# Performance work log

Hardware: AMD Instinct MI355X
Metric: run time of the kernel (lower is better)

Reference implementation:

```python
import jax, jax.numpy as jnp
import numpy as np

N_NODES = 50000
N_EDGES = 640000
NFEAT = 128
NHID = 128
BN_EPS = 1e-5
GIN_EPS = 0.0  # GINConv default eps


def setup_inputs() -> dict:
    key = jax.random.key(0)
    ks = jax.random.split(key, 8)
    x = jax.random.normal(ks[0], (N_NODES, NFEAT), dtype=jnp.float32)
    edge_index = jax.random.randint(ks[1], (2, N_EDGES), 0, N_NODES, dtype=jnp.int64)
    # xavier-uniform linears, zero bias (per weights_init); BN gamma=1, beta=0
    def xavier(k, fan_in, fan_out):
        a = float(np.sqrt(6.0 / (fan_in + fan_out)))
        return jax.random.uniform(k, (fan_in, fan_out), dtype=jnp.float32, minval=-a, maxval=a)
    W1 = xavier(ks[2], NFEAT, NHID)
    b1 = jnp.zeros((NHID,), dtype=jnp.float32)
    gamma = jnp.ones((NHID,), dtype=jnp.float32)
    beta = jnp.zeros((NHID,), dtype=jnp.float32)
    W2 = xavier(ks[3], NHID, NHID)
    b2 = jnp.zeros((NHID,), dtype=jnp.float32)
    return {"x": x, "edge_index": edge_index, "W1": W1, "b1": b1,
            "gamma": gamma, "beta": beta, "W2": W2, "b2": b2}


def reference(x, edge_index, W1, b1, gamma, beta, W2, b2):
    src, dst = edge_index[0], edge_index[1]
    # sparse neighbor sum-aggregation: agg[i] = sum_{(src->dst=i)} x[src]
    agg = jax.ops.segment_sum(x[src], dst, num_segments=x.shape[0])
    h = (1.0 + GIN_EPS) * x + agg
    # MLP: Linear -> ReLU -> BatchNorm1d (training-mode batch stats) -> Linear
    h = jax.nn.relu(h @ W1 + b1)
    mean = jnp.mean(h, axis=0)
    var = jnp.mean(jnp.square(h - mean), axis=0)  # biased var, as torch BN uses
    h = (h - mean) * jax.lax.rsqrt(var + BN_EPS) * gamma + beta
    return h @ W2 + b2
```

## Files before the change

kernel.cpp:

```cpp
#include <hip/hip_runtime.h>
#include <hip/hip_fp16.h>

#define NNODES 50000
#define NEDGES 640000
#define NF 128
#define XB 3125
#define WB 64
#define BINS 196
#define BINCAP 4096
#define P1B 625

typedef __attribute__((ext_vector_type(8))) _Float16 f16x8;
typedef __attribute__((ext_vector_type(4))) float f32x4;

__global__ __launch_bounds__(256) void k_prep(const float* __restrict__ x,
                                              const float* __restrict__ W1,
                                              const int* __restrict__ ei,
                                              unsigned short* __restrict__ xh,
                                              _Float16* __restrict__ wp1,
                                              int* __restrict__ gcursor,
                                              unsigned* __restrict__ binbuf,
                                              float* __restrict__ stats) {
  __shared__ int lcnt[BINS], lbase[BINS];
  const int bid = blockIdx.x, t = threadIdx.x;
  if (bid < XB) {
    int i = bid * 256 + t;
    const float4 a = ((const float4*)x)[2 * i];
    const float4 b = ((const float4*)x)[2 * i + 1];
    __half2 h0 = __float22half2_rn(make_float2(a.x, a.y));
    __half2 h1 = __float22half2_rn(make_float2(a.z, a.w));
    __half2 h2 = __float22half2_rn(make_float2(b.x, b.y));
    __half2 h3 = __float22half2_rn(make_float2(b.z, b.w));
    uint4 v;
    v.x = *(unsigned*)&h0; v.y = *(unsigned*)&h1;
    v.z = *(unsigned*)&h2; v.w = *(unsigned*)&h3;
    ((uint4*)xh)[i] = v;
    if (bid == 0) { stats[t] = 0.f; stats[256 + t] = 0.f; }
  } else if (bid < XB + WB) {
    int f = (bid - XB) * 256 + t;
    int j = f & 7, lane = (f >> 3) & 63, cf = (f >> 9) & 7, ks = f >> 12;
    int k = ks * 32 + ((lane >> 4) << 3) + j;
    int n = cf * 16 + (lane & 15);
    float w = W1[k * NF + n];
    _Float16 hi = (_Float16)w;
    _Float16 lo = (_Float16)(w - (float)hi);
    wp1[f] = hi;
    wp1[16384 + f] = lo;
  } else {
    const int e0 = (bid - (XB + WB)) * 1024;
    const int4 s4 = *(const int4*)(ei + e0 + 4 * t);
    const int4 d4 = *(const int4*)(ei + NEDGES + e0 + 4 * t);
    if (t < BINS) lcnt[t] = 0;
    __syncthreads();
    atomicAdd(&lcnt[d4.x >> 8], 1);
    atomicAdd(&lcnt[d4.y >> 8], 1);
    atomicAdd(&lcnt[d4.z >> 8], 1);
    atomicAdd(&lcnt[d4.w >> 8], 1);
    __syncthreads();
    if (t < BINS) {
      lbase[t] = atomicAdd(&gcursor[t], lcnt[t]);
      lcnt[t] = 0;
    }
    __syncthreads();
    {
      int bin = d4.x >> 8;
      int idx = lbase[bin] + atomicAdd(&lcnt[bin], 1);
      if (idx < BINCAP) binbuf[bin * BINCAP + idx] = ((unsigned)(d4.x & 255) << 16) | (unsigned)s4.x;
    }
    {
      int bin = d4.y >> 8;
      int idx = lbase[bin] + atomicAdd(&lcnt[bin], 1);
      if (idx < BINCAP) binbuf[bin * BINCAP + idx] = ((unsigned)(d4.y & 255) << 16) | (unsigned)s4.y;
    }
    {
      int bin = d4.z >> 8;
      int idx = lbase[bin] + atomicAdd(&lcnt[bin], 1);
      if (idx < BINCAP) binbuf[bin * BINCAP + idx] = ((unsigned)(d4.z & 255) << 16) | (unsigned)s4.z;
    }
    {
      int bin = d4.w >> 8;
      int idx = lbase[bin] + atomicAdd(&lcnt[bin], 1);
      if (idx < BINCAP) binbuf[bin * BINCAP + idx] = ((unsigned)(d4.w & 255) << 16) | (unsigned)s4.w;
    }
  }
}

__global__ __launch_bounds__(256) void k_p2(const unsigned* __restrict__ binbuf,
                                            const int* __restrict__ gcursor,
                                            int* __restrict__ begdeg,
                                            unsigned short* __restrict__ slot) {
  __shared__ int cnt2[256], pst[256];
  __shared__ unsigned short stg[BINCAP];
  const int t = threadIdx.x;
  const int b = blockIdx.x;
  const int base = b * BINCAP;
  const int nb = min(gcursor[b], BINCAP);
  unsigned pk[16];
#pragma unroll
  for (int ci = 0; ci < 16; ++ci) {
    int i = (ci << 8) + t;
    pk[ci] = (i < nb) ? binbuf[base + i] : 0xFFFFFFFFu;
  }
  cnt2[t] = 0;
  __syncthreads();
#pragma unroll
  for (int ci = 0; ci < 16; ++ci)
    if (pk[ci] != 0xFFFFFFFFu) atomicAdd(&cnt2[(int)(pk[ci] >> 16)], 1);
  __syncthreads();
  pst[t] = cnt2[t];
  __syncthreads();
  for (int d = 1; d < 256; d <<= 1) {
    int u = (t >= d) ? pst[t - d] : 0;
    __syncthreads();
    pst[t] += u;
    __syncthreads();
  }
  pst[t] -= cnt2[t];
  int node = (b << 8) + t;
  if (node < NNODES)
    begdeg[node] = ((base + pst[t]) << 8) | min(cnt2[t], 255);
  cnt2[t] = 0;
  __syncthreads();
#pragma unroll
  for (int ci = 0; ci < 16; ++ci)
    if (pk[ci] != 0xFFFFFFFFu) {
      int dl = (int)(pk[ci] >> 16);
      int pos = atomicAdd(&cnt2[dl], 1);
      stg[pst[dl] + pos] = (unsigned short)(pk[ci] & 0xffffu);
    }
  __syncthreads();
  for (int i = t; i < nb; i += 256) slot[base + i] = stg[i];
}

__device__ inline void add8h(float* a, uint4 v) {
  const __half2* p = (const __half2*)&v;
#pragma unroll
  for (int q = 0; q < 4; ++q) {
    float2 f = __half22float2(p[q]);
    a[2 * q] += f.x;
    a[2 * q + 1] += f.y;
  }
}

__global__ __launch_bounds__(256) void k_gather(const unsigned short* __restrict__ xh,
                                                const int* __restrict__ begdeg,
                                                const unsigned short* __restrict__ slot,
                                                _Float16* __restrict__ h) {
  const int t = threadIdx.x;
  const int wv = t >> 6, l = t & 63;
  const int node = blockIdx.x * 4 + wv;
  if (node >= NNODES) return;
  const int cg = (l & 15) << 3;
  const int e = l >> 4;
  const int bd = begdeg[node];
  const int beg = bd >> 8;
  const int end = beg + (bd & 255);
  float a[8] = {0.f, 0.f, 0.f, 0.f, 0.f, 0.f, 0.f, 0.f};
  float b[8] = {0.f, 0.f, 0.f, 0.f, 0.f, 0.f, 0.f, 0.f};
  int j = beg + e;
  for (; j + 4 < end; j += 8) {
    const uint4 v0 = *(const uint4*)(xh + (size_t)slot[j] * NF + cg);
    const uint4 v1 = *(const uint4*)(xh + (size_t)slot[j + 4] * NF + cg);
    add8h(a, v0);
    add8h(b, v1);
  }
  if (j < end) {
    const uint4 v0 = *(const uint4*)(xh + (size_t)slot[j] * NF + cg);
    add8h(a, v0);
  }
#pragma unroll
  for (int q = 0; q < 8; ++q) a[q] += b[q];
#pragma unroll
  for (int q = 0; q < 8; ++q) {
    a[q] += __shfl_xor(a[q], 16);
    a[q] += __shfl_xor(a[q], 32);
  }
  if (e == 0) {
    const uint4 sv = *(const uint4*)(xh + (size_t)node * NF + cg);
    add8h(a, sv);
    f16x8 o;
#pragma unroll
    for (int q = 0; q < 8; ++q) o[q] = (_Float16)a[q];
    *(f16x8*)(h + (size_t)node * NF + cg) = o;
  }
}

template <int MODE>
__global__ __launch_bounds__(256, 2) void k_gemm(const _Float16* __restrict__ A,
                                                 const _Float16* __restrict__ wprep,
                                                 const float* __restrict__ bias,
                                                 float* __restrict__ stats,
                                                 _Float16* __restrict__ outh,
                                                 float* __restrict__ outf) {
  __shared__ _Float16 wl[32768];
  __shared__ float red[2][4][128];

  const int t = threadIdx.x;
  const int wv = t >> 6;
  const int l = t & 63;
  const int wrow0 = blockIdx.x * 128 + wv * 16;

  f16x8 areg[2][4];
#pragma unroll
  for (int m = 0; m < 2; ++m) {
    const int arow = wrow0 + m * 64 + (l & 15);
    const bool okA = arow < NNODES;
#pragma unroll
    for (int ks = 0; ks < 4; ++ks) {
      if (okA) {
        areg[m][ks] = *(const f16x8*)(A + (size_t)arow * NF + ks * 32 + ((l >> 4) << 3));
      } else {
        areg[m][ks] = (f16x8){};
      }
    }
  }

  const float4* src = (const float4*)wprep;
#pragma unroll
  for (int it = 0; it < 16; ++it) {
    ((float4*)wl)[it * 256 + t] = src[it * 256 + t];
  }
  __syncthreads();

  f32x4 acc[2][8];
#pragma unroll
  for (int m = 0; m < 2; ++m)
#pragma unroll
    for (int cf = 0; cf < 8; ++cf) acc[m][cf] = (f32x4){0.f, 0.f, 0.f, 0.f};

#pragma unroll
  for (int ks = 0; ks < 4; ++ks) {
#pragma unroll
    for (int cf = 0; cf < 8; ++cf) {
      const int fo = (((ks * 8 + cf) << 6) + l) << 3;
      f16x8 bh = *(const f16x8*)(wl + fo);
      f16x8 bl = *(const f16x8*)(wl + 16384 + fo);
#pragma unroll
      for (int m = 0; m < 2; ++m) {
        acc[m][cf] = __builtin_amdgcn_mfma_f32_16x16x32_f16(areg[m][ks], bh, acc[m][cf], 0, 0, 0);
        acc[m][cf] = __builtin_amdgcn_mfma_f32_16x16x32_f16(areg[m][ks], bl, acc[m][cf], 0, 0, 0);
      }
    }
  }

  const int col16 = l & 15;
  const int rg = l >> 4;
  float bl_[8];
#pragma unroll
  for (int cf = 0; cf < 8; ++cf) bl_[cf] = bias[cf * 16 + col16];

  if (MODE == 0) {
    float cs[8], cq[8];
#pragma unroll
    for (int cf = 0; cf < 8; ++cf) { cs[cf] = 0.f; cq[cf] = 0.f; }
#pragma unroll
    for (int m = 0; m < 2; ++m)
#pragma unroll
      for (int cf = 0; cf < 8; ++cf) {
#pragma unroll
        for (int r = 0; r < 4; ++r) {
          int row = wrow0 + m * 64 + rg * 4 + r;
          if (row < NNODES) {
            float v = fmaxf(acc[m][cf][r] + bl_[cf], 0.f);
            outh[(size_t)row * NF + cf * 16 + col16] = (_Float16)v;
            cs[cf] += v;
            cq[cf] += v * v;
          }
        }
      }
#pragma unroll
    for (int cf = 0; cf < 8; ++cf) {
      cs[cf] += __shfl_xor(cs[cf], 16); cs[cf] += __shfl_xor(cs[cf], 32);
      cq[cf] += __shfl_xor(cq[cf], 16); cq[cf] += __shfl_xor(cq[cf], 32);
    }
    if (l < 16) {
#pragma unroll
      for (int cf = 0; cf < 8; ++cf) {
        red[0][wv][cf * 16 + l] = cs[cf];
        red[1][wv][cf * 16 + l] = cq[cf];
      }
    }
    __syncthreads();
    if (t < 128) {
      float s = red[0][0][t] + red[0][1][t] + red[0][2][t] + red[0][3][t];
      float q = red[1][0][t] + red[1][1][t] + red[1][2][t] + red[1][3][t];
      unsafeAtomicAdd(stats + t, s);
      unsafeAtomicAdd(stats + 128 + t, q);
    }
  } else {
#pragma unroll
    for (int m = 0; m < 2; ++m)
#pragma unroll
      for (int cf = 0; cf < 8; ++cf) {
#pragma unroll
        for (int r = 0; r < 4; ++r) {
          int row = wrow0 + m * 64 + rg * 4 + r;
          if (row < NNODES)
            outf[(size_t)row * NF + cf * 16 + col16] = acc[m][cf][r] + bl_[cf];
        }
      }
  }
}

__global__ __launch_bounds__(1024) void k_bnfold(const float* __restrict__ stats,
                                                 const float* __restrict__ gamma,
                                                 const float* __restrict__ beta,
                                                 const float* __restrict__ W2,
                                                 const float* __restrict__ b2,
                                                 _Float16* __restrict__ wp2,
                                                 float* __restrict__ b2p) {
  __shared__ float sc_s[128], sh_s[128];
  __shared__ float part[8][128];
  const int t = threadIdx.x;
  if (t < 128) {
    const float inv = 1.0f / (float)NNODES;
    float mean = stats[t] * inv;
    float var = stats[128 + t] * inv - mean * mean;
    var = fmaxf(var, 0.f);
    float sc = gamma[t] * rsqrtf(var + 1e-5f);
    sc_s[t] = sc;
    sh_s[t] = beta[t] - mean * sc;
  }
  __syncthreads();
#pragma unroll
  for (int it = 0; it < 16; ++it) {
    int f = it * 1024 + t;
    int j = f & 7, lane = (f >> 3) & 63, cf = (f >> 9) & 7, ks = f >> 12;
    int k = ks * 32 + ((lane >> 4) << 3) + j;
    int n = cf * 16 + (lane & 15);
    float w = sc_s[k] * W2[k * NF + n];
    _Float16 hi = (_Float16)w;
    _Float16 lo = (_Float16)(w - (float)hi);
    wp2[f] = hi;
    wp2[16384 + f] = lo;
  }
  {
    const int col = t & 127, ch = t >> 7;
    float s = 0.f;
    for (int k = ch * 16; k < ch * 16 + 16; ++k) s += sh_s[k] * W2[k * NF + col];
    part[ch][col] = s;
  }
  __syncthreads();
  if (t < 128) {
    float v = b2[t];
#pragma unroll
    for (int c = 0; c < 8; ++c) v += part[c][t];
    b2p[t] = v;
  }
}

extern "C" void kernel_launch(void* const* d_in, const int* in_sizes, int n_in,
                              void* d_out, int out_size, void* d_ws, size_t ws_size,
                              hipStream_t stream) {
  const float* x     = (const float*)d_in[0];
  const int*   ei    = (const int*)d_in[1];
  const float* W1    = (const float*)d_in[2];
  const float* b1    = (const float*)d_in[3];
  const float* gamma = (const float*)d_in[4];
  const float* beta  = (const float*)d_in[5];
  const float* W2    = (const float*)d_in[6];
  const float* b2    = (const float*)d_in[7];
  float* out = (float*)d_out;

  _Float16* h = (_Float16*)d_out;

  float*          stats   = (float*)d_ws;
  _Float16*       wp1     = (_Float16*)(stats + 512);
  _Float16*       wp2     = wp1 + 32768;
  float*          b2p     = (float*)(wp2 + 32768);
  int*            gcursor = (int*)(b2p + 128);
  int*            begdeg  = gcursor + 256;
  unsigned*       binbuf  = (unsigned*)(begdeg + 50176);
  unsigned short* slot    = (unsigned short*)(binbuf + BINS * BINCAP);
  unsigned short* xh      = slot + BINS * BINCAP;
  _Float16*       h1      = (_Float16*)(xh + (size_t)NNODES * NF);

  hipMemsetAsync(gcursor, 0, 256 * sizeof(int), stream);
  k_prep   <<<XB + WB + P1B, 256, 0, stream>>>(x, W1, ei, xh, wp1, gcursor, binbuf, stats);
  k_p2     <<<BINS, 256, 0, stream>>>(binbuf, gcursor, begdeg, slot);
  k_gather <<<(NNODES + 3) / 4, 256, 0, stream>>>(xh, begdeg, slot, h);
  k_gemm<0><<<(NNODES + 127) / 128, 256, 0, stream>>>(h, wp1, b1, stats, h1, nullptr);
  k_bnfold <<<1, 1024, 0, stream>>>(stats, gamma, beta, W2, b2, wp2, b2p);
  k_gemm<1><<<(NNODES + 127) / 128, 256, 0, stream>>>(h1, wp2, b2p, nullptr, nullptr, out);
}
```

Baseline: 105.3 us.

## Replace global-atomic edge binning with count/scan/scatter passes; parallelize BN fold

The edge binning step no longer reserves space per bin with global atomics on a shared cursor. It now writes per-block bin counts, runs a per-bin exclusive scan across blocks in a new kernel, and then scatters the edges in a third kernel using the precomputed offsets. This removes the memset and global atomic contention, and it makes the bin order deterministic. The cost is two extra kernel launches and a second read of the edge indices. The BN-fold kernel is also split from one 1024-thread block into 17 blocks, which spreads the weight repacking across more compute units.

```diff
diff --git a/kernel.cpp b/kernel.cpp
--- a/kernel.cpp
+++ b/kernel.cpp
@@ -8,7 +8,8 @@
 #define WB 64
 #define BINS 196
 #define BINCAP 4096
-#define P1B 625
+#define P1AB 313
+#define EPB 2048
 
 typedef __attribute__((ext_vector_type(8))) _Float16 f16x8;
 typedef __attribute__((ext_vector_type(4))) float f32x4;
@@ -18,10 +19,9 @@
                                               const int* __restrict__ ei,
                                               unsigned short* __restrict__ xh,
                                               _Float16* __restrict__ wp1,
-                                              int* __restrict__ gcursor,
-                                              unsigned* __restrict__ binbuf,
+                                              int* __restrict__ cnt,
                                               float* __restrict__ stats) {
-  __shared__ int lcnt[BINS], lbase[BINS];
+  __shared__ int lcnt[BINS];
   const int bid = blockIdx.x, t = threadIdx.x;
   if (bid < XB) {
     int i = bid * 256 + t;
@@ -47,46 +47,75 @@
     wp1[f] = hi;
     wp1[16384 + f] = lo;
   } else {
-    const int e0 = (bid - (XB + WB)) * 1024;
-    const int4 s4 = *(const int4*)(ei + e0 + 4 * t);
-    const int4 d4 = *(const int4*)(ei + NEDGES + e0 + 4 * t);
+    const int blk = bid - (XB + WB);
+    const int e0 = blk * EPB;
+    const bool full = (e0 + EPB <= NEDGES);
     if (t < BINS) lcnt[t] = 0;
     __syncthreads();
-    atomicAdd(&lcnt[d4.x >> 8], 1);
-    atomicAdd(&lcnt[d4.y >> 8], 1);
-    atomicAdd(&lcnt[d4.z >> 8], 1);
-    atomicAdd(&lcnt[d4.w >> 8], 1);
-    __syncthreads();
-    if (t < BINS) {
-      lbase[t] = atomicAdd(&gcursor[t], lcnt[t]);
-      lcnt[t] = 0;
-    }
-    __syncthreads();
-    {
-      int bin = d4.x >> 8;
-      int idx = lbase[bin] + atomicAdd(&lcnt[bin], 1);
-      if (idx < BINCAP) binbuf[bin * BINCAP + idx] = ((unsigned)(d4.x & 255) << 16) | (unsigned)s4.x;
-    }
-    {
-      int bin = d4.y >> 8;
-      int idx = lbase[bin] + atomicAdd(&lcnt[bin], 1);
-      if (idx < BINCAP) binbuf[bin * BINCAP + idx] = ((unsigned)(d4.y & 255) << 16) | (unsigned)s4.y;
-    }
-    {
-      int bin = d4.z >> 8;
-      int idx = lbase[bin] + atomicAdd(&lcnt[bin], 1);
-      if (idx < BINCAP) binbuf[bin * BINCAP + idx] = ((unsigned)(d4.z & 255) << 16) | (unsigned)s4.z;
-    }
-    {
-      int bin = d4.w >> 8;
-      int idx = lbase[bin] + atomicAdd(&lcnt[bin], 1);
-      if (idx < BINCAP) binbuf[bin * BINCAP + idx] = ((unsigned)(d4.w & 255) << 16) | (unsigned)s4.w;
-    }
-  }
+    const int4 d0 = *(const int4*)(ei + NEDGES + e0 + 4 * t);
+    atomicAdd(&lcnt[d0.x >> 8], 1);
+    atomicAdd(&lcnt[d0.y >> 8], 1);
+    atomicAdd(&lcnt[d0.z >> 8], 1);
+    atomicAdd(&lcnt[d0.w >> 8], 1);
+    if (full) {
+      const int4 d1 = *(const int4*)(ei + NEDGES + e0 + 1024 + 4 * t);
+      atomicAdd(&lcnt[d1.x >> 8], 1);
+      atomicAdd(&lcnt[d1.y >> 8], 1);
+      atomicAdd(&lcnt[d1.z >> 8], 1);
+      atomicAdd(&lcnt[d1.w >> 8], 1);
+    }
+    __syncthreads();
+    if (t < BINS) cnt[blk * BINS + t] = lcnt[t];
+  }
+}
+
+__global__ __launch_bounds__(512) void k_p1b(const int* __restrict__ cnt,
+                                             int* __restrict__ base,
+                                             int* __restrict__ gtot) {
+  __shared__ int s[512];
+  const int t = threadIdx.x, b = blockIdx.x;
+  const int v = (t < P1AB) ? cnt[t * BINS + b] : 0;
+  s[t] = v;
+  __syncthreads();
+  for (int d = 1; d < 512; d <<= 1) {
+    int u = (t >= d) ? s[t - d] : 0;
+    __syncthreads();
+    s[t] += u;
+    __syncthreads();
+  }
+  if (t < P1AB) base[t * BINS + b] = s[t] - v;
+  if (t == 511) gtot[b] = s[511];
+}
+
+__global__ __launch_bounds__(256) void k_p1c(const int* __restrict__ ei,
+                                             const int* __restrict__ base,
+                                             unsigned* __restrict__ binbuf) {
+  __shared__ int lcur[BINS];
+  const int t = threadIdx.x, blk = blockIdx.x;
+  const int e0 = blk * EPB;
+  const bool full = (e0 + EPB <= NEDGES);
+  if (t < BINS) lcur[t] = base[blk * BINS + t];
+  __syncthreads();
+  const int4 s0 = *(const int4*)(ei + e0 + 4 * t);
+  const int4 d0 = *(const int4*)(ei + NEDGES + e0 + 4 * t);
+#define SCAT(ss, dd)                                                             \
+  {                                                                              \
+    int bin = (dd) >> 8;                                                         \
+    int pos = atomicAdd(&lcur[bin], 1);                                          \
+    if (pos < BINCAP)                                                            \
+      binbuf[bin * BINCAP + pos] = ((unsigned)((dd) & 255) << 16) | (unsigned)(ss); \
+  }
+  SCAT(s0.x, d0.x); SCAT(s0.y, d0.y); SCAT(s0.z, d0.z); SCAT(s0.w, d0.w);
+  if (full) {
+    const int4 s1 = *(const int4*)(ei + e0 + 1024 + 4 * t);
+    const int4 d1 = *(const int4*)(ei + NEDGES + e0 + 1024 + 4 * t);
+    SCAT(s1.x, d1.x); SCAT(s1.y, d1.y); SCAT(s1.z, d1.z); SCAT(s1.w, d1.w);
+  }
+#undef SCAT
 }
 
 __global__ __launch_bounds__(256) void k_p2(const unsigned* __restrict__ binbuf,
-                                            const int* __restrict__ gcursor,
+                                            const int* __restrict__ gtot,
                                             int* __restrict__ begdeg,
                                             unsigned short* __restrict__ slot) {
   __shared__ int cnt2[256], pst[256];
@@ -94,7 +123,7 @@
   const int t = threadIdx.x;
   const int b = blockIdx.x;
   const int base = b * BINCAP;
-  const int nb = min(gcursor[b], BINCAP);
+  const int nb = min(gtot[b], BINCAP);
   unsigned pk[16];
 #pragma unroll
   for (int ci = 0; ci < 16; ++ci) {
@@ -302,16 +331,16 @@
   }
 }
 
-__global__ __launch_bounds__(1024) void k_bnfold(const float* __restrict__ stats,
-                                                 const float* __restrict__ gamma,
-                                                 const float* __restrict__ beta,
-                                                 const float* __restrict__ W2,
-                                                 const float* __restrict__ b2,
-                                                 _Float16* __restrict__ wp2,
-                                                 float* __restrict__ b2p) {
+__global__ __launch_bounds__(256) void k_fold(const float* __restrict__ stats,
+                                              const float* __restrict__ gamma,
+                                              const float* __restrict__ beta,
+                                              const float* __restrict__ W2,
+                                              const float* __restrict__ b2,
+                                              _Float16* __restrict__ wp2,
+                                              float* __restrict__ b2p) {
   __shared__ float sc_s[128], sh_s[128];
-  __shared__ float part[8][128];
-  const int t = threadIdx.x;
+  __shared__ float part[2][128];
+  const int t = threadIdx.x, bb = blockIdx.x;
   if (t < 128) {
     const float inv = 1.0f / (float)NNODES;
     float mean = stats[t] * inv;
@@ -322,30 +351,26 @@
     sh_s[t] = beta[t] - mean * sc;
   }
   __syncthreads();
-#pragma unroll
-  for (int it = 0; it < 16; ++it) {
-    int f = it * 1024 + t;
-    int j = f & 7, lane = (f >> 3) & 63, cf = (f >> 9) & 7, ks = f >> 12;
-    int k = ks * 32 + ((lane >> 4) << 3) + j;
-    int n = cf * 16 + (lane & 15);
-    float w = sc_s[k] * W2[k * NF + n];
-    _Float16 hi = (_Float16)w;
-    _Float16 lo = (_Float16)(w - (float)hi);
-    wp2[f] = hi;
-    wp2[16384 + f] = lo;
-  }
-  {
+  if (bb < 16) {
+#pragma unroll
+    for (int it = 0; it < 4; ++it) {
+      int f = bb * 1024 + it * 256 + t;
+      int j = f & 7, lane = (f >> 3) & 63, cf = (f >> 9) & 7, ks = f >> 12;
+      int k = ks * 32 + ((lane >> 4) << 3) + j;
+      int n = cf * 16 + (lane & 15);
+      float w = sc_s[k] * W2[k * NF + n];
+      _Float16 hi = (_Float16)w;
+      _Float16 lo = (_Float16)(w - (float)hi);
+      wp2[f] = hi;
+      wp2[16384 + f] = lo;
+    }
+  } else {
     const int col = t & 127, ch = t >> 7;
     float s = 0.f;
-    for (int k = ch * 16; k < ch * 16 + 16; ++k) s += sh_s[k] * W2[k * NF + col];
+    for (int k = ch * 64; k < ch * 64 + 64; ++k) s += sh_s[k] * W2[k * NF + col];
     part[ch][col] = s;
-  }
-  __syncthreads();
-  if (t < 128) {
-    float v = b2[t];
-#pragma unroll
-    for (int c = 0; c < 8; ++c) v += part[c][t];
-    b2p[t] = v;
+    __syncthreads();
+    if (t < 128) b2p[t] = b2[t] + part[0][t] + part[1][t];
   }
 }
 
@@ -364,22 +389,25 @@
 
   _Float16* h = (_Float16*)d_out;
 
-  float*          stats   = (float*)d_ws;
-  _Float16*       wp1     = (_Float16*)(stats + 512);
-  _Float16*       wp2     = wp1 + 32768;
-  float*          b2p     = (float*)(wp2 + 32768);
-  int*            gcursor = (int*)(b2p + 128);
-  int*            begdeg  = gcursor + 256;
-  unsigned*       binbuf  = (unsigned*)(begdeg + 50176);
-  unsigned short* slot    = (unsigned short*)(binbuf + BINS * BINCAP);
-  unsigned short* xh      = slot + BINS * BINCAP;
-  _Float16*       h1      = (_Float16*)(xh + (size_t)NNODES * NF);
-
-  hipMemsetAsync(gcursor, 0, 256 * sizeof(int), stream);
-  k_prep   <<<XB + WB + P1B, 256, 0, stream>>>(x, W1, ei, xh, wp1, gcursor, binbuf, stats);
-  k_p2     <<<BINS, 256, 0, stream>>>(binbuf, gcursor, begdeg, slot);
+  float*          stats  = (float*)d_ws;
+  _Float16*       wp1    = (_Float16*)(stats + 512);
+  _Float16*       wp2    = wp1 + 32768;
+  float*          b2p    = (float*)(wp2 + 32768);
+  int*            cnt    = (int*)(b2p + 128);
+  int*            basep  = cnt + 61376;
+  int*            gtot   = basep + 61376;
+  int*            begdeg = gtot + 256;
+  unsigned*       binbuf = (unsigned*)(begdeg + 50176);
+  unsigned short* slot   = (unsigned short*)(binbuf + BINS * BINCAP);
+  unsigned short* xh     = slot + BINS * BINCAP;
+  _Float16*       h1     = (_Float16*)(xh + (size_t)NNODES * NF);
+
+  k_prep   <<<XB + WB + P1AB, 256, 0, stream>>>(x, W1, ei, xh, wp1, cnt, stats);
+  k_p1b    <<<BINS, 512, 0, stream>>>(cnt, basep, gtot);
+  k_p1c    <<<P1AB, 256, 0, stream>>>(ei, basep, binbuf);
+  k_p2     <<<BINS, 256, 0, stream>>>(binbuf, gtot, begdeg, slot);
   k_gather <<<(NNODES + 3) / 4, 256, 0, stream>>>(xh, begdeg, slot, h);
   k_gemm<0><<<(NNODES + 127) / 128, 256, 0, stream>>>(h, wp1, b1, stats, h1, nullptr);
-  k_bnfold <<<1, 1024, 0, stream>>>(stats, gamma, beta, W2, b2, wp2, b2p);
+  k_fold   <<<17, 256, 0, stream>>>(stats, gamma, beta, W2, b2, wp2, b2p);
   k_gemm<1><<<(NNODES + 127) / 128, 256, 0, stream>>>(h1, wp2, b2p, nullptr, nullptr, out);
 }
```

New measurement: 90.56 us. 14.0% less time.

## Replace atomic edge binning with count-scan-scatter cooperative sort and fold weight prep into GEMMs

Applied to the files above, without the earlier changes.

Edge binning now counts per-block bin histograms in the prep kernel, then runs a single cooperative kernel. That kernel scans the counts, scatters edges to fixed per-block offsets and does the per-bin CSR build, separated by grid syncs. This replaces the global atomic cursors, the memset and the separate k_p2 launch. The W1/W2 fp16 hi/lo packing and the BatchNorm fold are moved into each GEMM block, which removes the standalone prep work and the single-block k_bnfold launch. In exchange, every GEMM block redundantly converts the full weight matrix from fp32, and the second GEMM also recomputes the folded bias serially. The change also depends on cooperative launch and grid-wide barriers.

```diff
diff --git a/kernel.cpp b/kernel.cpp
--- a/kernel.cpp
+++ b/kernel.cpp
@@ -1,27 +1,27 @@
 #include <hip/hip_runtime.h>
 #include <hip/hip_fp16.h>
+#include <hip/hip_cooperative_groups.h>
+
+namespace cg = cooperative_groups;
 
 #define NNODES 50000
 #define NEDGES 640000
 #define NF 128
 #define XB 3125
-#define WB 64
 #define BINS 196
 #define BINCAP 4096
-#define P1B 625
+#define P1AB 250
+#define EPB 2560
 
 typedef __attribute__((ext_vector_type(8))) _Float16 f16x8;
 typedef __attribute__((ext_vector_type(4))) float f32x4;
 
 __global__ __launch_bounds__(256) void k_prep(const float* __restrict__ x,
-                                              const float* __restrict__ W1,
                                               const int* __restrict__ ei,
                                               unsigned short* __restrict__ xh,
-                                              _Float16* __restrict__ wp1,
-                                              int* __restrict__ gcursor,
-                                              unsigned* __restrict__ binbuf,
+                                              int* __restrict__ cnt,
                                               float* __restrict__ stats) {
-  __shared__ int lcnt[BINS], lbase[BINS];
+  __shared__ int lcnt[BINS];
   const int bid = blockIdx.x, t = threadIdx.x;
   if (bid < XB) {
     int i = bid * 256 + t;
@@ -36,100 +36,101 @@
     v.z = *(unsigned*)&h2; v.w = *(unsigned*)&h3;
     ((uint4*)xh)[i] = v;
     if (bid == 0) { stats[t] = 0.f; stats[256 + t] = 0.f; }
-  } else if (bid < XB + WB) {
-    int f = (bid - XB) * 256 + t;
-    int j = f & 7, lane = (f >> 3) & 63, cf = (f >> 9) & 7, ks = f >> 12;
-    int k = ks * 32 + ((lane >> 4) << 3) + j;
-    int n = cf * 16 + (lane & 15);
-    float w = W1[k * NF + n];
-    _Float16 hi = (_Float16)w;
-    _Float16 lo = (_Float16)(w - (float)hi);
-    wp1[f] = hi;
-    wp1[16384 + f] = lo;
   } else {
-    const int e0 = (bid - (XB + WB)) * 1024;
-    const int4 s4 = *(const int4*)(ei + e0 + 4 * t);
-    const int4 d4 = *(const int4*)(ei + NEDGES + e0 + 4 * t);
+    const int blk = bid - XB;
+    const int e0 = blk * EPB;
     if (t < BINS) lcnt[t] = 0;
     __syncthreads();
-    atomicAdd(&lcnt[d4.x >> 8], 1);
-    atomicAdd(&lcnt[d4.y >> 8], 1);
-    atomicAdd(&lcnt[d4.z >> 8], 1);
-    atomicAdd(&lcnt[d4.w >> 8], 1);
-    __syncthreads();
-    if (t < BINS) {
-      lbase[t] = atomicAdd(&gcursor[t], lcnt[t]);
-      lcnt[t] = 0;
-    }
-    __syncthreads();
-    {
-      int bin = d4.x >> 8;
-      int idx = lbase[bin] + atomicAdd(&lcnt[bin], 1);
-      if (idx < BINCAP) binbuf[bin * BINCAP + idx] = ((unsigned)(d4.x & 255) << 16) | (unsigned)s4.x;
-    }
-    {
-      int bin = d4.y >> 8;
-      int idx = lbase[bin] + atomicAdd(&lcnt[bin], 1);
-      if (idx < BINCAP) binbuf[bin * BINCAP + idx] = ((unsigned)(d4.y & 255) << 16) | (unsigned)s4.y;
-    }
-    {
-      int bin = d4.z >> 8;
-      int idx = lbase[bin] + atomicAdd(&lcnt[bin], 1);
-      if (idx < BINCAP) binbuf[bin * BINCAP + idx] = ((unsigned)(d4.z & 255) << 16) | (unsigned)s4.z;
-    }
-    {
-      int bin = d4.w >> 8;
-      int idx = lbase[bin] + atomicAdd(&lcnt[bin], 1);
-      if (idx < BINCAP) binbuf[bin * BINCAP + idx] = ((unsigned)(d4.w & 255) << 16) | (unsigned)s4.w;
-    }
-  }
-}
-
-__global__ __launch_bounds__(256) void k_p2(const unsigned* __restrict__ binbuf,
-                                            const int* __restrict__ gcursor,
-                                            int* __restrict__ begdeg,
-                                            unsigned short* __restrict__ slot) {
+    for (int i = t; i < EPB; i += 256)
+      atomicAdd(&lcnt[ei[NEDGES + e0 + i] >> 8], 1);
+    __syncthreads();
+    if (t < BINS) cnt[blk * BINS + t] = lcnt[t];
+  }
+}
+
+__global__ __launch_bounds__(256) void k_sort(const int* __restrict__ ei,
+                                              const int* __restrict__ cnt,
+                                              int* __restrict__ base,
+                                              unsigned* __restrict__ binbuf,
+                                              int* __restrict__ begdeg,
+                                              unsigned short* __restrict__ slot) {
+  __shared__ int sbuf[256];
+  __shared__ int lcur[BINS];
+  __shared__ int nb_sh;
   __shared__ int cnt2[256], pst[256];
   __shared__ unsigned short stg[BINCAP];
-  const int t = threadIdx.x;
-  const int b = blockIdx.x;
-  const int base = b * BINCAP;
-  const int nb = min(gcursor[b], BINCAP);
-  unsigned pk[16];
-#pragma unroll
-  for (int ci = 0; ci < 16; ++ci) {
-    int i = (ci << 8) + t;
-    pk[ci] = (i < nb) ? binbuf[base + i] : 0xFFFFFFFFu;
-  }
-  cnt2[t] = 0;
-  __syncthreads();
-#pragma unroll
-  for (int ci = 0; ci < 16; ++ci)
-    if (pk[ci] != 0xFFFFFFFFu) atomicAdd(&cnt2[(int)(pk[ci] >> 16)], 1);
-  __syncthreads();
-  pst[t] = cnt2[t];
-  __syncthreads();
-  for (int d = 1; d < 256; d <<= 1) {
-    int u = (t >= d) ? pst[t - d] : 0;
-    __syncthreads();
-    pst[t] += u;
-    __syncthreads();
-  }
-  pst[t] -= cnt2[t];
-  int node = (b << 8) + t;
-  if (node < NNODES)
-    begdeg[node] = ((base + pst[t]) << 8) | min(cnt2[t], 255);
-  cnt2[t] = 0;
-  __syncthreads();
-#pragma unroll
-  for (int ci = 0; ci < 16; ++ci)
-    if (pk[ci] != 0xFFFFFFFFu) {
-      int dl = (int)(pk[ci] >> 16);
-      int pos = atomicAdd(&cnt2[dl], 1);
-      stg[pst[dl] + pos] = (unsigned short)(pk[ci] & 0xffffu);
-    }
-  __syncthreads();
-  for (int i = t; i < nb; i += 256) slot[base + i] = stg[i];
+  cg::grid_group grid = cg::this_grid();
+  const int t = threadIdx.x, b = blockIdx.x;
+
+  if (b < BINS) {
+    int v = (t < P1AB) ? cnt[t * BINS + b] : 0;
+    sbuf[t] = v;
+    __syncthreads();
+    for (int d = 1; d < 256; d <<= 1) {
+      int u = (t >= d) ? sbuf[t - d] : 0;
+      __syncthreads();
+      sbuf[t] += u;
+      __syncthreads();
+    }
+    if (t < P1AB) base[t * BINS + b] = sbuf[t] - v;
+    if (t == 255) nb_sh = sbuf[255];
+  }
+  grid.sync();
+
+  {
+    const int e0 = b * EPB;
+    if (t < BINS) lcur[t] = base[b * BINS + t];
+    __syncthreads();
+    for (int i = t; i < EPB; i += 256) {
+      int s = ei[e0 + i];
+      int d = ei[NEDGES + e0 + i];
+      int bin = d >> 8;
+      int pos = atomicAdd(&lcur[bin], 1);
+      if (pos < BINCAP)
+        binbuf[bin * BINCAP + pos] = ((unsigned)(d & 255) << 16) | (unsigned)s;
+    }
+  }
+  grid.sync();
+
+  if (b < BINS) {
+    const int basei = b * BINCAP;
+    const int nb = min(nb_sh, BINCAP);
+    unsigned pk[16];
+#pragma unroll
+    for (int ci = 0; ci < 16; ++ci) {
+      int i = (ci << 8) + t;
+      pk[ci] = (i < nb) ? binbuf[basei + i] : 0xFFFFFFFFu;
+    }
+    cnt2[t] = 0;
+    __syncthreads();
+#pragma unroll
+    for (int ci = 0; ci < 16; ++ci)
+      if (pk[ci] != 0xFFFFFFFFu) atomicAdd(&cnt2[(int)(pk[ci] >> 16)], 1);
+    __syncthreads();
+    pst[t] = cnt2[t];
+    __syncthreads();
+    for (int d = 1; d < 256; d <<= 1) {
+      int u = (t >= d) ? pst[t - d] : 0;
+      __syncthreads();
+      pst[t] += u;
+      __syncthreads();
+    }
+    pst[t] -= cnt2[t];
+    int node = (b << 8) + t;
+    if (node < NNODES)
+      begdeg[node] = ((basei + pst[t]) << 8) | min(cnt2[t], 255);
+    cnt2[t] = 0;
+    __syncthreads();
+#pragma unroll
+    for (int ci = 0; ci < 16; ++ci)
+      if (pk[ci] != 0xFFFFFFFFu) {
+        int dl = (int)(pk[ci] >> 16);
+        int pos = atomicAdd(&cnt2[dl], 1);
+        stg[pst[dl] + pos] = (unsigned short)(pk[ci] & 0xffffu);
+      }
+    __syncthreads();
+    for (int i = t; i < nb; i += 256) slot[basei + i] = stg[i];
+  }
 }
 
 __device__ inline void add8h(float* a, uint4 v) {
@@ -150,7 +151,7 @@
   const int wv = t >> 6, l = t & 63;
   const int node = blockIdx.x * 4 + wv;
   if (node >= NNODES) return;
-  const int cg = (l & 15) << 3;
+  const int cg_ = (l & 15) << 3;
   const int e = l >> 4;
   const int bd = begdeg[node];
   const int beg = bd >> 8;
@@ -159,13 +160,13 @@
   float b[8] = {0.f, 0.f, 0.f, 0.f, 0.f, 0.f, 0.f, 0.f};
   int j = beg + e;
   for (; j + 4 < end; j += 8) {
-    const uint4 v0 = *(const uint4*)(xh + (size_t)slot[j] * NF + cg);
-    const uint4 v1 = *(const uint4*)(xh + (size_t)slot[j + 4] * NF + cg);
+    const uint4 v0 = *(const uint4*)(xh + (size_t)slot[j] * NF + cg_);
+    const uint4 v1 = *(const uint4*)(xh + (size_t)slot[j + 4] * NF + cg_);
     add8h(a, v0);
     add8h(b, v1);
   }
   if (j < end) {
-    const uint4 v0 = *(const uint4*)(xh + (size_t)slot[j] * NF + cg);
+    const uint4 v0 = *(const uint4*)(xh + (size_t)slot[j] * NF + cg_);
     add8h(a, v0);
   }
 #pragma unroll
@@ -176,24 +177,27 @@
     a[q] += __shfl_xor(a[q], 32);
   }
   if (e == 0) {
-    const uint4 sv = *(const uint4*)(xh + (size_t)node * NF + cg);
+    const uint4 sv = *(const uint4*)(xh + (size_t)node * NF + cg_);
     add8h(a, sv);
     f16x8 o;
 #pragma unroll
     for (int q = 0; q < 8; ++q) o[q] = (_Float16)a[q];
-    *(f16x8*)(h + (size_t)node * NF + cg) = o;
+    *(f16x8*)(h + (size_t)node * NF + cg_) = o;
   }
 }
 
 template <int MODE>
 __global__ __launch_bounds__(256, 2) void k_gemm(const _Float16* __restrict__ A,
-                                                 const _Float16* __restrict__ wprep,
+                                                 const float* __restrict__ W,
                                                  const float* __restrict__ bias,
+                                                 const float* __restrict__ gamma,
+                                                 const float* __restrict__ beta,
                                                  float* __restrict__ stats,
                                                  _Float16* __restrict__ outh,
                                                  float* __restrict__ outf) {
   __shared__ _Float16 wl[32768];
   __shared__ float red[2][4][128];
+  __shared__ float scs[128], shs[128], b2sh[128];
 
   const int t = threadIdx.x;
   const int wv = t >> 6;
@@ -215,12 +219,48 @@
     }
   }
 
-  const float4* src = (const float4*)wprep;
-#pragma unroll
-  for (int it = 0; it < 16; ++it) {
-    ((float4*)wl)[it * 256 + t] = src[it * 256 + t];
+  if (MODE == 1) {
+    if (t < 128) {
+      const float inv = 1.0f / (float)NNODES;
+      float mean = stats[t] * inv;
+      float var = fmaxf(stats[128 + t] * inv - mean * mean, 0.f);
+      float sc = gamma[t] * rsqrtf(var + 1e-5f);
+      scs[t] = sc;
+      shs[t] = beta[t] - mean * sc;
+    }
+    __syncthreads();
+  }
+
+#pragma unroll
+  for (int oct = 0; oct < 8; ++oct) {
+    int f8 = oct * 256 + t;
+    int ks = f8 >> 9, cf = (f8 >> 6) & 7, lane = f8 & 63;
+    int k0 = ks * 32 + ((lane >> 4) << 3);
+    int n = cf * 16 + (lane & 15);
+    f16x8 hi, lo;
+#pragma unroll
+    for (int j = 0; j < 8; ++j) {
+      float w = W[(k0 + j) * NF + n];
+      if (MODE == 1) w *= scs[k0 + j];
+      _Float16 h_ = (_Float16)w;
+      hi[j] = h_;
+      lo[j] = (_Float16)(w - (float)h_);
+    }
+    *(f16x8*)(wl + f8 * 8) = hi;
+    *(f16x8*)(wl + 16384 + f8 * 8) = lo;
+  }
+
+  if (MODE == 1) {
+    const int col = t & 127, half = t >> 7;
+    float s = 0.f;
+    for (int k = half * 64; k < half * 64 + 64; ++k) s += shs[k] * W[k * NF + col];
+    red[0][half][col] = s;
   }
   __syncthreads();
+  if (MODE == 1) {
+    if (t < 128) b2sh[t] = bias[t] + red[0][0][t] + red[0][1][t];
+    __syncthreads();
+  }
 
   f32x4 acc[2][8];
 #pragma unroll
@@ -247,7 +287,8 @@
   const int rg = l >> 4;
   float bl_[8];
 #pragma unroll
-  for (int cf = 0; cf < 8; ++cf) bl_[cf] = bias[cf * 16 + col16];
+  for (int cf = 0; cf < 8; ++cf)
+    bl_[cf] = (MODE == 0) ? bias[cf * 16 + col16] : b2sh[cf * 16 + col16];
 
   if (MODE == 0) {
     float cs[8], cq[8];
@@ -273,6 +314,7 @@
       cs[cf] += __shfl_xor(cs[cf], 16); cs[cf] += __shfl_xor(cs[cf], 32);
       cq[cf] += __shfl_xor(cq[cf], 16); cq[cf] += __shfl_xor(cq[cf], 32);
     }
+    __syncthreads();
     if (l < 16) {
 #pragma unroll
       for (int cf = 0; cf < 8; ++cf) {
@@ -299,53 +341,6 @@
             outf[(size_t)row * NF + cf * 16 + col16] = acc[m][cf][r] + bl_[cf];
         }
       }
-  }
-}
-
-__global__ __launch_bounds__(1024) void k_bnfold(const float* __restrict__ stats,
-                                                 const float* __restrict__ gamma,
-                                                 const float* __restrict__ beta,
-                                                 const float* __restrict__ W2,
-                                                 const float* __restrict__ b2,
-                                                 _Float16* __restrict__ wp2,
-                                                 float* __restrict__ b2p) {
-  __shared__ float sc_s[128], sh_s[128];
-  __shared__ float part[8][128];
-  const int t = threadIdx.x;
-  if (t < 128) {
-    const float inv = 1.0f / (float)NNODES;
-    float mean = stats[t] * inv;
-    float var = stats[128 + t] * inv - mean * mean;
-    var = fmaxf(var, 0.f);
-    float sc = gamma[t] * rsqrtf(var + 1e-5f);
-    sc_s[t] = sc;
-    sh_s[t] = beta[t] - mean * sc;
-  }
-  __syncthreads();
-#pragma unroll
-  for (int it = 0; it < 16; ++it) {
-    int f = it * 1024 + t;
-    int j = f & 7, lane = (f >> 3) & 63, cf = (f >> 9) & 7, ks = f >> 12;
-    int k = ks * 32 + ((lane >> 4) << 3) + j;
-    int n = cf * 16 + (lane & 15);
-    float w = sc_s[k] * W2[k * NF + n];
-    _Float16 hi = (_Float16)w;
-    _Float16 lo = (_Float16)(w - (float)hi);
-    wp2[f] = hi;
-    wp2[16384 + f] = lo;
-  }
-  {
-    const int col = t & 127, ch = t >> 7;
-    float s = 0.f;
-    for (int k = ch * 16; k < ch * 16 + 16; ++k) s += sh_s[k] * W2[k * NF + col];
-    part[ch][col] = s;
-  }
-  __syncthreads();
-  if (t < 128) {
-    float v = b2[t];
-#pragma unroll
-    for (int c = 0; c < 8; ++c) v += part[c][t];
-    b2p[t] = v;
   }
 }
 
@@ -364,22 +359,27 @@
 
   _Float16* h = (_Float16*)d_out;
 
-  float*          stats   = (float*)d_ws;
-  _Float16*       wp1     = (_Float16*)(stats + 512);
-  _Float16*       wp2     = wp1 + 32768;
-  float*          b2p     = (float*)(wp2 + 32768);
-  int*            gcursor = (int*)(b2p + 128);
-  int*            begdeg  = gcursor + 256;
-  unsigned*       binbuf  = (unsigned*)(begdeg + 50176);
-  unsigned short* slot    = (unsigned short*)(binbuf + BINS * BINCAP);
-  unsigned short* xh      = slot + BINS * BINCAP;
-  _Float16*       h1      = (_Float16*)(xh + (size_t)NNODES * NF);
-
-  hipMemsetAsync(gcursor, 0, 256 * sizeof(int), stream);
-  k_prep   <<<XB + WB + P1B, 256, 0, stream>>>(x, W1, ei, xh, wp1, gcursor, binbuf, stats);
-  k_p2     <<<BINS, 256, 0, stream>>>(binbuf, gcursor, begdeg, slot);
+  float*          stats  = (float*)d_ws;
+  int*            cnt    = (int*)(stats + 512);
+  int*            basep  = cnt + 49152;
+  int*            begdeg = basep + 49152;
+  unsigned*       binbuf = (unsigned*)(begdeg + 50176);
+  unsigned short* slot   = (unsigned short*)(binbuf + BINS * BINCAP);
+  unsigned short* xh     = slot + BINS * BINCAP;
+  _Float16*       h1     = (_Float16*)(xh + (size_t)NNODES * NF);
+
+  k_prep<<<XB + P1AB, 256, 0, stream>>>(x, ei, xh, cnt, stats);
+
+  {
+    void* args[] = {(void*)&ei, (void*)&cnt, (void*)&basep,
+                    (void*)&binbuf, (void*)&begdeg, (void*)&slot};
+    hipLaunchCooperativeKernel((const void*)k_sort, dim3(P1AB), dim3(256),
+                               args, 0, stream);
+  }
+
   k_gather <<<(NNODES + 3) / 4, 256, 0, stream>>>(xh, begdeg, slot, h);
-  k_gemm<0><<<(NNODES + 127) / 128, 256, 0, stream>>>(h, wp1, b1, stats, h1, nullptr);
-  k_bnfold <<<1, 1024, 0, stream>>>(stats, gamma, beta, W2, b2, wp2, b2p);
-  k_gemm<1><<<(NNODES + 127) / 128, 256, 0, stream>>>(h1, wp2, b2p, nullptr, nullptr, out);
-}
+  k_gemm<0><<<(NNODES + 127) / 128, 256, 0, stream>>>(h, W1, b1, nullptr, nullptr,
+                                                      stats, h1, nullptr);
+  k_gemm<1><<<(NNODES + 127) / 128, 256, 0, stream>>>(h1, W2, b2, gamma, beta,
+                                                      stats, nullptr, out);
+}
```

New measurement: 169.1 us. 60.5% more time.
